# Kernel optimization log

Hardware: AMD Instinct MI355X
Metric: run time of the kernel (lower is better)

The kernel has to match this reference:

```python
import jax, jax.numpy as jnp
import numpy as np

B, S, F_DIM, FILT = 4096, 41, 128, 128
EPS_BN = 1e-5
EPS_SQ = 1e-21


def squash(v):
    n = jnp.linalg.norm(v, axis=-1, keepdims=True)
    return (1.0 - 1.0 / (jnp.exp(n) + EPS_SQ)) * (v / (n + EPS_SQ))


def position_linear(x, Wstack, bstack, window):
    # x: [B,S,F]; Wstack: [S, window*F, FILT]; bstack: [S, FILT]
    p = window // 2
    Bq, Sq, Fq = x.shape
    xp = jnp.pad(x, ((0, 0), (p, p), (0, 0)))
    idx = jnp.arange(Sq)[:, None] + jnp.arange(window)[None, :]  # [S, window]
    xw = xp[:, idx, :].reshape(Bq, Sq, window * Fq)
    return jax.nn.relu(jnp.einsum('bsf,sfo->bso', xw, Wstack) + bstack[None])


def batchnorm(x, g, b, axes):
    mu = jnp.mean(x, axis=axes, keepdims=True)
    var = jnp.var(x, axis=axes, keepdims=True)
    shape = [1] * x.ndim
    shape[1] = x.shape[1]
    return (x - mu) * jax.lax.rsqrt(var + EPS_BN) * g.reshape(shape) + b.reshape(shape)


def conv1d(x, w, groups=1):
    # x: [N,C,L], w: [O, C//groups, K], padding same (k=3, pad=1)
    return jax.lax.conv_general_dilated(
        x, w, window_strides=(1,), padding=[(1, 1)],
        dimension_numbers=('NCH', 'OIH', 'NCH'), feature_group_count=groups)


def setup_inputs() -> dict:
    key = jax.random.key(0)
    ks = jax.random.split(key, 16)
    sc = lambda fan_in: 1.0 / np.sqrt(fan_in)
    d = {}
    d['x'] = jax.random.randint(ks[0], (B, S), 0, 4, dtype=jnp.int32)
    d['emb'] = jax.random.normal(ks[1], (4, F_DIM), dtype=jnp.float32)
    for i, w in enumerate([3, 5, 7]):
        fin = w * F_DIM
        d[f'W{w}'] = jax.random.uniform(ks[2 + i], (S, fin, FILT), jnp.float32, -sc(fin), sc(fin))
        d[f'b{w}'] = jnp.zeros((S, FILT), jnp.float32)
    d['conv1_w'] = jax.random.uniform(ks[5], (64, 41, 3), jnp.float32, -sc(41 * 3), sc(41 * 3))
    d['conv1_b'] = jnp.zeros((64,), jnp.float32)
    d['bn_g'] = jnp.ones((64,), jnp.float32)
    d['bn_b'] = jnp.zeros((64,), jnp.float32)
    d['caps_w'] = jax.random.uniform(ks[6], (64, 32, 3), jnp.float32, -sc(32 * 3), sc(32 * 3))
    d['caps_b'] = jnp.zeros((64,), jnp.float32)
    d['route_W'] = jax.random.normal(ks[7], (2, 64, F_DIM), jnp.float32)
    d['route_b'] = jnp.zeros((2, 64, 1), jnp.float32)
    d['fc1_w'] = jax.random.uniform(ks[8], (F_DIM, 64), jnp.float32, -sc(F_DIM), sc(F_DIM))
    d['bn1_g'] = jnp.ones((2,), jnp.float32)
    d['bn1_b'] = jnp.zeros((2,), jnp.float32)
    d['fc2_w'] = jax.random.uniform(ks[9], (64, 32), jnp.float32, -sc(64), sc(64))
    d['bn2_g'] = jnp.ones((2,), jnp.float32)
    d['bn2_b'] = jnp.zeros((2,), jnp.float32)
    d['fc3_w'] = jax.random.uniform(ks[10], (32, 1), jnp.float32, -sc(32), sc(32))
    return d


def reference(x, emb, W3, b3, W5, b5, W7, b7, conv1_w, conv1_b, bn_g, bn_b,
              caps_w, caps_b, route_W, route_b,
              fc1_w, bn1_g, bn1_b, fc2_w, bn2_g, bn2_b, fc3_w):
    h = emb[x]                                    # [B,41,128]
    h = position_linear(h, W3, b3, 3)
    h = position_linear(h, W5, b5, 5)
    h = position_linear(h, W7, b7, 7)             # [B,41,128]
    h = conv1d(h, conv1_w) + conv1_b[None, :, None]  # [B,64,128]
    h = jax.nn.relu(batchnorm(h, bn_g, bn_b, axes=(0, 2)))
    h = conv1d(h, caps_w, groups=2) + caps_b[None, :, None]
    h = squash(h)                                 # [B,64,128]
    # Routing layer
    u = h[:, None, :, :] * route_W[None]          # [B,2,64,128]
    c = jnp.sum(u * u, axis=-1, keepdims=True) / jnp.sqrt(128.0)  # [B,2,64,1]
    c = jax.nn.softmax(c, axis=-1)                # softmax over size-1 axis -> ones
    c = c + route_b[None]
    s = squash(jnp.sum(u * c, axis=-2))           # [B,2,128]
    # FC head
    pair = s[:, :, None, :] + s[:, None, :, :]    # [B,2,2,128]
    y = jnp.max(pair, axis=1)                     # [B,2,128]
    y = jax.nn.relu(batchnorm(y @ fc1_w, bn1_g, bn1_b, axes=(0, 2)))
    y = jax.nn.relu(batchnorm(y @ fc2_w, bn2_g, bn2_b, axes=(0, 2)))
    y = jax.nn.sigmoid(y @ fc3_w)                 # [B,2,1]
    return jnp.max(y, axis=1)                     # [B,1]
```

## Files before the change

kernel.cpp:

```cpp
#include <hip/hip_runtime.h>
#include <cstdint>

typedef unsigned short u16;
typedef unsigned int   u32;
typedef __attribute__((ext_vector_type(8))) short bf16x8;
typedef __attribute__((ext_vector_type(4))) float f32x4;

#define DEVFN static __device__ __forceinline__

constexpr int B  = 4096;
constexpr int SQ = 41;

DEVFN float bf2f(u16 v) { return __uint_as_float(((u32)v) << 16); }
DEVFN u16 f2bf(float f) {
  u32 u = __float_as_uint(f);
  u += 0x7fffu + ((u >> 16) & 1u);
  return (u16)(u >> 16);
}
DEVFN u32 pack2(float a, float b) { return (u32)f2bf(a) | ((u32)f2bf(b) << 16); }

DEVFN void gload16(const void* g, void* l) {
  __builtin_amdgcn_global_load_lds(
      (const __attribute__((address_space(1))) unsigned int*)g,
      (__attribute__((address_space(3))) unsigned int*)l, 16, 0, 0);
}

__global__ void k_pack(const float* __restrict__ cw, const float* __restrict__ cpw,
                       const float* __restrict__ rW, const float* __restrict__ rb,
                       u16* __restrict__ wpk, u16* __restrict__ cpk,
                       u16* __restrict__ rwp) {
  int i = blockIdx.x * 256 + threadIdx.x;
  if (i < 12288) {
    int tt = i >> 12, rem = i & 4095, o = rem >> 6, c = rem & 63;
    float v = (c < 41) ? cw[(o * 41 + c) * 3 + tt] : 0.f;
    wpk[(tt * 64 + o) * 64 + (c ^ ((o & 7) << 3))] = f2bf(v);
  } else if (i < 18432) {
    int k = i - 12288;
    int tt = k >> 11, rem = k & 2047, o = rem >> 5, c = rem & 31;
    cpk[(tt * 64 + o) * 32 + (c ^ ((o & 3) << 3))] = f2bf(cpw[(o * 32 + c) * 3 + tt]);
  } else if (i < 34816) {
    int k = i - 18432;
    rwp[k] = f2bf(rW[k] * (1.f + rb[k >> 7]));
  }
}

__global__ void k_combo(const int* __restrict__ x, int* __restrict__ combo) {
  int i = blockIdx.x * 256 + threadIdx.x;
  if (i >= B * SQ) return;
  int b = i / SQ, s = i - b * SQ;
  const int* xb = x + b * SQ;
  int d0 = (s > 0) ? xb[s - 1] : 4;
  int d1 = xb[s];
  int d2 = (s < SQ - 1) ? xb[s + 1] : 4;
  combo[i] = d0 * 25 + d1 * 5 + d2;
}

__global__ void k_gmat(const float* __restrict__ emb, const float* __restrict__ W3,
                       float* __restrict__ G) {
  int s = blockIdx.x / 3, ww = blockIdx.x % 3;
  int o = threadIdx.x;
  const float* Ws = W3 + ((size_t)s * 384 + ww * 128) * 128;
  float a0 = 0.f, a1 = 0.f, a2 = 0.f, a3 = 0.f;
  for (int f = 0; f < 128; ++f) {
    float wg = Ws[(size_t)f * 128 + o];
    a0 = fmaf(emb[f], wg, a0);
    a1 = fmaf(emb[128 + f], wg, a1);
    a2 = fmaf(emb[256 + f], wg, a2);
    a3 = fmaf(emb[384 + f], wg, a3);
  }
  float* Gp = G + ((size_t)(s * 3 + ww) * 5) * 128 + o;
  Gp[0] = a0; Gp[128] = a1; Gp[256] = a2; Gp[384] = a3; Gp[512] = 0.f;
}

__global__ void k_t1(const float* __restrict__ G, const float* __restrict__ b3,
                     u16* __restrict__ t1b) {
  int i = blockIdx.x * 256 + threadIdx.x;
  int f = i & 127, v = (i >> 7) & 127, s = i >> 14;
  u16 out = 0;
  if (v < 125) {
    int d0 = v / 25, r = v % 25;
    int d1 = r / 5, d2 = r % 5;
    float acc = b3[s * 128 + f]
        + G[((size_t)(s * 3 + 0) * 5 + d0) * 128 + f]
        + G[((size_t)(s * 3 + 1) * 5 + d1) * 128 + f]
        + G[((size_t)(s * 3 + 2) * 5 + d2) * 128 + f];
    out = f2bf(fmaxf(acc, 0.f));
  }
  t1b[i] = out;
}

__global__ __launch_bounds__(256) void k_w5t(const float* __restrict__ W5,
                                             u16* __restrict__ w5t) {
  __shared__ float tile[64][65];
  const int sw = blockIdx.z;
  const int s = sw / 5, w = sw % 5;
  const int f0 = blockIdx.x * 64;
  const int o0 = blockIdx.y * 64;
  const int t = threadIdx.x;
  const float* Ws = W5 + ((size_t)s * 640 + w * 128) * 128;
  #pragma unroll
  for (int i = 0; i < 16; ++i) {
    int idx = t + i * 256;
    int fl = idx >> 6, ol = idx & 63;
    tile[fl][ol] = Ws[(size_t)(f0 + fl) * 128 + o0 + ol];
  }
  __syncthreads();
  #pragma unroll
  for (int i = 0; i < 16; ++i) {
    int idx = t + i * 256;
    int ol = idx >> 6, fl = idx & 63;
    w5t[((size_t)sw * 128 + o0 + ol) * 128 + f0 + fl] = f2bf(tile[fl][ol]);
  }
}

__global__ __launch_bounds__(256) void k_t2_mfma(const u16* __restrict__ t1b,
                                                 const u16* __restrict__ w5t,
                                                 u16* __restrict__ t2) {
  __shared__ u16 As[2][8192];
  __shared__ u16 Bs[2][8192];
  const int sw = blockIdx.x;
  const int s = sw / 5, w5 = sw % 5;
  const int tw = s + w5 - 2;
  if (tw < 0 || tw >= SQ) return;
  const int t = threadIdx.x;
  const int lane = t & 63, w = t >> 6;
  const int wr = w >> 1, wc = w & 1;
  const int lcol = lane & 15, qk = lane >> 4;

  const u16* abase = t1b + (size_t)tw * 128 * 128;
  const u16* bbase = w5t + (size_t)sw * 128 * 128;
  #pragma unroll
  for (int h = 0; h < 2; ++h) {
    #pragma unroll
    for (int it = 0; it < 4; ++it) {
      const int L = it * 4096 + t * 16;
      const int r = L >> 7, g = (L >> 4) & 7;
      const int gs = g ^ (r & 7);
      gload16(abase + (size_t)r * 128 + h * 64 + gs * 8,
              (char*)As[h] + it * 4096 + w * 1024);
      gload16(bbase + (size_t)r * 128 + h * 64 + gs * 8,
              (char*)Bs[h] + it * 4096 + w * 1024);
    }
  }
  __syncthreads();

  f32x4 acc[4][4];
  #pragma unroll
  for (int i = 0; i < 4; ++i)
    #pragma unroll
    for (int j = 0; j < 4; ++j) acc[i][j] = (f32x4){0.f, 0.f, 0.f, 0.f};

  #pragma unroll
  for (int h = 0; h < 2; ++h) {
    #pragma unroll
    for (int kk = 0; kk < 2; ++kk) {
      const int gk = kk * 4 + qk;
      bf16x8 av[4], bv[4];
      #pragma unroll
      for (int m = 0; m < 4; ++m) {
        const int zr = wr * 64 + m * 16 + lcol;
        av[m] = *reinterpret_cast<const bf16x8*>(&As[h][zr * 64 + ((gk ^ (zr & 7)) << 3)]);
      }
      #pragma unroll
      for (int n = 0; n < 4; ++n) {
        const int br = wc * 64 + n * 16 + lcol;
        bv[n] = *reinterpret_cast<const bf16x8*>(&Bs[h][br * 64 + ((gk ^ (br & 7)) << 3)]);
      }
      #pragma unroll
      for (int m = 0; m < 4; ++m)
        #pragma unroll
        for (int n = 0; n < 4; ++n)
          acc[m][n] = __builtin_amdgcn_mfma_f32_16x16x32_bf16(av[m], bv[n], acc[m][n], 0, 0, 0);
    }
  }

  u16* dst = t2 + (size_t)sw * 125 * 128;
  const int rq = (lane >> 4) * 4;
  #pragma unroll
  for (int n = 0; n < 4; ++n) {
    const int o = wc * 64 + n * 16 + lcol;
    #pragma unroll
    for (int m = 0; m < 4; ++m) {
      #pragma unroll
      for (int rg = 0; rg < 4; ++rg) {
        const int row = wr * 64 + m * 16 + rq + rg;
        if (row < 125) dst[(size_t)row * 128 + o] = f2bf(acc[m][n][rg]);
      }
    }
  }
}

__global__ __launch_bounds__(256) void k_h2(const u16* __restrict__ t2,
                                            const int* __restrict__ combo,
                                            const float* __restrict__ b5,
                                            u16* __restrict__ h2) {
  const int i = blockIdx.x * 256 + threadIdx.x;
  const int o8 = (i & 15) * 8;
  const int rid = i >> 4;
  const int s = rid >> 12, b = rid & 4095;
  float acc[8];
  {
    float4 b0 = *reinterpret_cast<const float4*>(b5 + s * 128 + o8);
    float4 b1 = *reinterpret_cast<const float4*>(b5 + s * 128 + o8 + 4);
    acc[0] = b0.x; acc[1] = b0.y; acc[2] = b0.z; acc[3] = b0.w;
    acc[4] = b1.x; acc[5] = b1.y; acc[6] = b1.z; acc[7] = b1.w;
  }
  const int* cb = combo + b * SQ;
  #pragma unroll
  for (int ww = 0; ww < 5; ++ww) {
    const int t = s + ww - 2;
    if (0 <= t && t < SQ) {
      const int c = cb[t];
      uint4 raw = *reinterpret_cast<const uint4*>(
          t2 + ((size_t)(s * 5 + ww) * 125 + c) * 128 + o8);
      acc[0] += __uint_as_float(raw.x << 16);
      acc[1] += __uint_as_float(raw.x & 0xffff0000u);
      acc[2] += __uint_as_float(raw.y << 16);
      acc[3] += __uint_as_float(raw.y & 0xffff0000u);
      acc[4] += __uint_as_float(raw.z << 16);
      acc[5] += __uint_as_float(raw.z & 0xffff0000u);
      acc[6] += __uint_as_float(raw.w << 16);
      acc[7] += __uint_as_float(raw.w & 0xffff0000u);
    }
  }
  uint4 pk;
  pk.x = pack2(fmaxf(acc[0], 0.f), fmaxf(acc[1], 0.f));
  pk.y = pack2(fmaxf(acc[2], 0.f), fmaxf(acc[3], 0.f));
  pk.z = pack2(fmaxf(acc[4], 0.f), fmaxf(acc[5], 0.f));
  pk.w = pack2(fmaxf(acc[6], 0.f), fmaxf(acc[7], 0.f));
  *reinterpret_cast<uint4*>(h2 + ((size_t)b * SQ + s) * 128 + o8) = pk;
}

__global__ __launch_bounds__(256) void k_w7t(const float* __restrict__ W7,
                                             u16* __restrict__ w7t) {
  __shared__ float tile[64][65];
  const int s = blockIdx.z;
  const int k0 = blockIdx.x * 64;
  const int o0 = blockIdx.y * 64;
  const int t = threadIdx.x;
  #pragma unroll
  for (int i = 0; i < 16; ++i) {
    int idx = t + i * 256;
    int kl = idx >> 6, ol = idx & 63;
    tile[kl][ol] = W7[((size_t)s * 896 + k0 + kl) * 128 + o0 + ol];
  }
  __syncthreads();
  #pragma unroll
  for (int i = 0; i < 16; ++i) {
    int idx = t + i * 256;
    int ol = idx >> 6, kl = idx & 63;
    w7t[((size_t)s * 128 + o0 + ol) * 896 + k0 + kl] = f2bf(tile[kl][ol]);
  }
}

__global__ __launch_bounds__(256) void k_gemm7_mfma(const u16* __restrict__ h2,
                                                    const u16* __restrict__ w7t,
                                                    const float* __restrict__ b7,
                                                    u16* __restrict__ h3) {
  __shared__ u16 As[2][8192];
  __shared__ u16 Bs[2][8192];
  const int s  = blockIdx.y;
  const int b0 = blockIdx.x * 128;
  const int t  = threadIdx.x;
  const int lane = t & 63, w = t >> 6;
  const int wr = w >> 1, wc = w & 1;
  const int lcol = lane & 15, qk = lane >> 4;

  f32x4 acc[4][4];
  #pragma unroll
  for (int i = 0; i < 4; ++i)
    #pragma unroll
    for (int j = 0; j < 4; ++j) acc[i][j] = (f32x4){0.f, 0.f, 0.f, 0.f};

  const u16* wbase = w7t + (size_t)s * 128 * 896;

  auto stage = [&](int kt, int bi) -> int {
    const int k0 = kt * 64;
    const int ww = k0 >> 7, tr = s + ww - 3, kf0 = k0 & 127;
    int issued = 0;
    if (0 <= tr && tr < SQ) {
      #pragma unroll
      for (int it = 0; it < 4; ++it) {
        const int L = it * 4096 + t * 16;
        const int r = L >> 7;
        const int g = (L >> 4) & 7;
        const int gs = g ^ (r & 7);
        gload16(h2 + ((size_t)(b0 + r) * SQ + tr) * 128 + kf0 + gs * 8,
                (char*)As[bi] + it * 4096 + w * 1024);
      }
      issued += 4;
    } else {
      #pragma unroll
      for (int it = 0; it < 4; ++it)
        *reinterpret_cast<uint4*>((char*)As[bi] + it * 4096 + t * 16) =
            make_uint4(0u, 0u, 0u, 0u);
    }
    #pragma unroll
    for (int it = 0; it < 4; ++it) {
      const int L = it * 4096 + t * 16;
      const int o = L >> 7;
      const int g = (L >> 4) & 7;
      const int gs = g ^ (o & 7);
      gload16(wbase + (size_t)o * 896 + k0 + gs * 8,
              (char*)Bs[bi] + it * 4096 + w * 1024);
    }
    return issued + 4;
  };

  stage(0, 0);

  for (int kt = 0; kt < 14; ++kt) {
    const int cur = kt & 1;
    int ni = 0;
    if (kt < 13) ni = stage(kt + 1, cur ^ 1);
    if (ni == 8)      asm volatile("s_waitcnt vmcnt(8) lgkmcnt(0)" ::: "memory");
    else if (ni == 4) asm volatile("s_waitcnt vmcnt(4) lgkmcnt(0)" ::: "memory");
    else              asm volatile("s_waitcnt vmcnt(0) lgkmcnt(0)" ::: "memory");
    __builtin_amdgcn_sched_barrier(0);
    __builtin_amdgcn_s_barrier();
    __builtin_amdgcn_sched_barrier(0);

    const u16* Ac = As[cur];
    const u16* Bc = Bs[cur];
    #pragma unroll
    for (int kk = 0; kk < 2; ++kk) {
      const int gk = kk * 4 + qk;
      bf16x8 av[4], bv[4];
      #pragma unroll
      for (int m = 0; m < 4; ++m) {
        const int zr = wr * 64 + m * 16 + lcol;
        av[m] = *reinterpret_cast<const bf16x8*>(Ac + zr * 64 + ((gk ^ (zr & 7)) << 3));
      }
      #pragma unroll
      for (int n = 0; n < 4; ++n) {
        const int br = wc * 64 + n * 16 + lcol;
        bv[n] = *reinterpret_cast<const bf16x8*>(Bc + br * 64 + ((gk ^ (br & 7)) << 3));
      }
      #pragma unroll
      for (int m = 0; m < 4; ++m)
        #pragma unroll
        for (int n = 0; n < 4; ++n)
          acc[m][n] = __builtin_amdgcn_mfma_f32_16x16x32_bf16(av[m], bv[n], acc[m][n], 0, 0, 0);
    }
    __builtin_amdgcn_sched_barrier(0);
    __builtin_amdgcn_s_barrier();
  }

  const int rq = (lane >> 4) * 4;
  #pragma unroll
  for (int n = 0; n < 4; ++n) {
    const int o = wc * 64 + n * 16 + lcol;
    const float bias = b7[s * 128 + o];
    #pragma unroll
    for (int m = 0; m < 4; ++m) {
      #pragma unroll
      for (int rg = 0; rg < 4; ++rg) {
        const int row = b0 + wr * 64 + m * 16 + rq + rg;
        h3[((size_t)row * SQ + s) * 128 + o] = f2bf(fmaxf(acc[m][n][rg] + bias, 0.f));
      }
    }
  }
}

constexpr int NBC = 8;
__global__ __launch_bounds__(256) void k_conv1(const u16* __restrict__ h3,
                                               const u16* __restrict__ wpk,
                                               const float* __restrict__ cb,
                                               u16* __restrict__ c1T,
                                               float2* __restrict__ part) {
  __shared__ u16 zs[2][6144];
  __shared__ u16 zt[130 * 64];
  __shared__ u16 wl[3 * 64 * 64];
  __shared__ float2 red[4][64];
  const int b0 = blockIdx.x * NBC;
  const int t = threadIdx.x;
  const int lane = t & 63, wv = t >> 6;
  const int r = lane & 15, kq = (lane >> 4) * 8, q = lane >> 4;

  #pragma unroll
  for (int it = 0; it < 6; ++it)
    gload16(wpk + ((size_t)it * 256 + t) * 8, (char*)wl + it * 4096 + wv * 1024);
  #pragma unroll
  for (int it = 0; it < 3; ++it)
    gload16(h3 + (size_t)b0 * (SQ * 128) + ((size_t)it * 256 + t) * 8,
            (char*)zs[0] + it * 4096 + wv * 1024);
  if (t < 64) zt[t] = 0;
  else if (t < 128) zt[129 * 64 + t - 64] = 0;
  __syncthreads();

  for (int i = 0; i < NBC; ++i) {
    const int b = b0 + i;
    const int cur = i & 1;

    {
      const int l = t & 127, jb = (t >> 7) * 32;
      const int sw = ((l + 1) & 7) << 3;
      u16* dst = zt + (l + 1) * 64;
      const u16* srcz = zs[cur];
      #pragma unroll
      for (int j = 0; j < 32; ++j) {
        int c = (jb + j + l) & 63;
        dst[c ^ sw] = (c < 41) ? srcz[c * 128 + l] : (u16)0;
      }
    }
    if (i + 1 < NBC) {
      #pragma unroll
      for (int it = 0; it < 3; ++it)
        gload16(h3 + (size_t)(b + 1) * (SQ * 128) + ((size_t)it * 256 + t) * 8,
                (char*)zs[cur ^ 1] + it * 4096 + wv * 1024);
    }
    asm volatile("s_waitcnt lgkmcnt(0)" ::: "memory");
    __builtin_amdgcn_sched_barrier(0);
    __builtin_amdgcn_s_barrier();
    __builtin_amdgcn_sched_barrier(0);

    f32x4 acc[2][4];
    #pragma unroll
    for (int m = 0; m < 2; ++m)
      #pragma unroll
      for (int n = 0; n < 4; ++n) acc[m][n] = (f32x4){0.f, 0.f, 0.f, 0.f};
    #pragma unroll
    for (int tt = 0; tt < 3; ++tt) {
      #pragma unroll
      for (int kk = 0; kk < 2; ++kk) {
        const int kof = kk * 32 + kq;
        bf16x8 av[2], bv[4];
        #pragma unroll
        for (int m = 0; m < 2; ++m) {
          const int zr = wv * 32 + m * 16 + r + tt;
          av[m] = *reinterpret_cast<const bf16x8*>(zt + zr * 64 + (kof ^ ((zr & 7) << 3)));
        }
        #pragma unroll
        for (int n = 0; n < 4; ++n) {
          const int o = n * 16 + r;
          bv[n] = *reinterpret_cast<const bf16x8*>(wl + (tt * 64 + o) * 64 + (kof ^ ((o & 7) << 3)));
        }
        #pragma unroll
        for (int m = 0; m < 2; ++m)
          #pragma unroll
          for (int n = 0; n < 4; ++n)
            acc[m][n] = __builtin_amdgcn_mfma_f32_16x16x32_bf16(av[m], bv[n], acc[m][n], 0, 0, 0);
      }
    }

    u16* outb = c1T + (size_t)b * 8192;
    #pragma unroll
    for (int n = 0; n < 4; ++n) {
      const int o = n * 16 + r;
      const float bias = cb[o];
      float s1 = 0.f, s2 = 0.f;
      #pragma unroll
      for (int m = 0; m < 2; ++m) {
        #pragma unroll
        for (int rg = 0; rg < 4; ++rg) {
          float v = acc[m][n][rg] + bias;
          s1 += v; s2 += v * v;
          outb[(wv * 32 + m * 16 + q * 4 + rg) * 64 + o] = f2bf(v);
        }
      }
      s1 += __shfl_xor(s1, 16); s1 += __shfl_xor(s1, 32);
      s2 += __shfl_xor(s2, 16); s2 += __shfl_xor(s2, 32);
      if (lane < 16) red[wv][n * 16 + lane] = make_float2(s1, s2);
    }
    __syncthreads();
    if (t < 64) {
      float S = red[0][t].x + red[1][t].x + red[2][t].x + red[3][t].x;
      float Q = red[0][t].y + red[1][t].y + red[2][t].y + red[3][t].y;
      part[(size_t)t * B + b] = make_float2(S, Q);
    }
    __syncthreads();
  }
}

__global__ void k_bnfin(const float2* __restrict__ part, const float* __restrict__ g,
                        const float* __restrict__ bb, float* __restrict__ scale,
                        float* __restrict__ shift) {
  int o = blockIdx.x;
  float s = 0.f, q = 0.f;
  for (int i = threadIdx.x; i < B; i += 256) {
    float2 p = part[(size_t)o * B + i];
    s += p.x; q += p.y;
  }
  #pragma unroll
  for (int off = 32; off; off >>= 1) { s += __shfl_down(s, off); q += __shfl_down(q, off); }
  __shared__ float rs[4], rq[4];
  int wv = threadIdx.x >> 6, ln = threadIdx.x & 63;
  if (ln == 0) { rs[wv] = s; rq[wv] = q; }
  __syncthreads();
  if (threadIdx.x == 0) {
    float S = rs[0] + rs[1] + rs[2] + rs[3];
    float Q = rq[0] + rq[1] + rq[2] + rq[3];
    const float n = (float)B * 128.f;
    float mu = S / n, var = Q / n - mu * mu;
    float sc = g[o] * rsqrtf(var + 1e-5f);
    scale[o] = sc; shift[o] = bb[o] - mu * sc;
  }
}

constexpr int NB = 8;
__global__ __launch_bounds__(256) void k_caps(const u16* __restrict__ c1T,
                                              const float* __restrict__ scale,
                                              const float* __restrict__ shift,
                                              const u16* __restrict__ cpk,
                                              const float* __restrict__ cpb,
                                              const u16* __restrict__ rwp,
                                              const float* __restrict__ f1,
                                              float* __restrict__ y1,
                                              float2* __restrict__ ppy1) {
  __shared__ u16 zt[130 * 64];
  __shared__ u16 wl[3 * 64 * 32];
  __shared__ float f1l[128 * 64];
  __shared__ float red[4][64];
  __shared__ float fl[64];
  __shared__ float sc_s[64], sh_s[64];
  __shared__ float red2[4][2];
  __shared__ float yl[2][128];
  __shared__ float pt[128];
  const int b0 = blockIdx.x * NB;
  const int t = threadIdx.x;
  const int lane = t & 63, wv = t >> 6;
  const int r = lane & 15, kq = (lane >> 4) * 8, q = lane >> 4;
  float ysum = 0.f, ysq = 0.f;

  #pragma unroll
  for (int it = 0; it < 3; ++it)
    gload16(cpk + ((size_t)it * 256 + t) * 8, (char*)wl + it * 4096 + wv * 1024);
  #pragma unroll
  for (int it = 0; it < 8; ++it)
    gload16(f1 + ((size_t)it * 256 + t) * 4, (char*)f1l + it * 4096 + wv * 1024);
  if (t < 64) { sc_s[t] = scale[t]; sh_s[t] = shift[t]; }
  if (t < 64) zt[t] = 0;
  else if (t < 128) zt[129 * 64 + t - 64] = 0;

  uint4 raw[4], rawn[4];
  {
    const u16* src = c1T + (size_t)b0 * 8192;
    #pragma unroll
    for (int p = 0; p < 4; ++p)
      raw[p] = *reinterpret_cast<const uint4*>(src + ((size_t)t + p * 256) * 8);
  }

  for (int i = 0; i < NB; ++i) {
    const int b = b0 + i;
    __syncthreads();

    #pragma unroll
    for (int p = 0; p < 4; ++p) {
      int idx = t + p * 256;
      int l = idx >> 3, c0 = (idx & 7) * 8;
      float vv[8];
      vv[0] = __uint_as_float(raw[p].x << 16); vv[1] = __uint_as_float(raw[p].x & 0xffff0000u);
      vv[2] = __uint_as_float(raw[p].y << 16); vv[3] = __uint_as_float(raw[p].y & 0xffff0000u);
      vv[4] = __uint_as_float(raw[p].z << 16); vv[5] = __uint_as_float(raw[p].z & 0xffff0000u);
      vv[6] = __uint_as_float(raw[p].w << 16); vv[7] = __uint_as_float(raw[p].w & 0xffff0000u);
      float a0 = fmaxf(fmaf(vv[0], sc_s[c0 + 0], sh_s[c0 + 0]), 0.f);
      float a1 = fmaxf(fmaf(vv[1], sc_s[c0 + 1], sh_s[c0 + 1]), 0.f);
      float a2 = fmaxf(fmaf(vv[2], sc_s[c0 + 2], sh_s[c0 + 2]), 0.f);
      float a3 = fmaxf(fmaf(vv[3], sc_s[c0 + 3], sh_s[c0 + 3]), 0.f);
      float a4 = fmaxf(fmaf(vv[4], sc_s[c0 + 4], sh_s[c0 + 4]), 0.f);
      float a5 = fmaxf(fmaf(vv[5], sc_s[c0 + 5], sh_s[c0 + 5]), 0.f);
      float a6 = fmaxf(fmaf(vv[6], sc_s[c0 + 6], sh_s[c0 + 6]), 0.f);
      float a7 = fmaxf(fmaf(vv[7], sc_s[c0 + 7], sh_s[c0 + 7]), 0.f);
      uint4 pk;
      pk.x = pack2(a0, a1); pk.y = pack2(a2, a3);
      pk.z = pack2(a4, a5); pk.w = pack2(a6, a7);
      *reinterpret_cast<uint4*>(zt + (l + 1) * 64 + (c0 ^ (((l + 1) & 7) << 3))) = pk;
    }
    if (i + 1 < NB) {
      const u16* srcn = c1T + (size_t)(b + 1) * 8192;
      #pragma unroll
      for (int p = 0; p < 4; ++p)
        rawn[p] = *reinterpret_cast<const uint4*>(srcn + ((size_t)t + p * 256) * 8);
    }
    __syncthreads();

    f32x4 acc[2][4];
    #pragma unroll
    for (int m = 0; m < 2; ++m)
      #pragma unroll
      for (int n = 0; n < 4; ++n) acc[m][n] = (f32x4){0.f, 0.f, 0.f, 0.f};
    #pragma unroll
    for (int tt = 0; tt < 3; ++tt) {
      bf16x8 av[2][2], bv[4];
      #pragma unroll
      for (int m = 0; m < 2; ++m) {
        const int zr = wv * 32 + m * 16 + r + tt;
        const int sw = (zr & 7) << 3;
        av[m][0] = *reinterpret_cast<const bf16x8*>(zt + zr * 64 + (kq ^ sw));
        av[m][1] = *reinterpret_cast<const bf16x8*>(zt + zr * 64 + ((32 + kq) ^ sw));
      }
      #pragma unroll
      for (int n = 0; n < 4; ++n) {
        const int o = n * 16 + r;
        bv[n] = *reinterpret_cast<const bf16x8*>(wl + (tt * 64 + o) * 32 + (kq ^ ((o & 3) << 3)));
      }
      #pragma unroll
      for (int m = 0; m < 2; ++m)
        #pragma unroll
        for (int n = 0; n < 4; ++n)
          acc[m][n] = __builtin_amdgcn_mfma_f32_16x16x32_bf16(av[m][n >> 1], bv[n], acc[m][n], 0, 0, 0);
    }

    #pragma unroll
    for (int n = 0; n < 4; ++n) {
      const int o = n * 16 + r;
      const float bias = cpb[o];
      float s2 = 0.f;
      #pragma unroll
      for (int m = 0; m < 2; ++m) {
        #pragma unroll
        for (int rg = 0; rg < 4; ++rg) {
          float v = acc[m][n][rg] + bias;
          acc[m][n][rg] = v;
          s2 += v * v;
        }
      }
      s2 += __shfl_xor(s2, 16); s2 += __shfl_xor(s2, 32);
      if (lane < 16) red[wv][n * 16 + lane] = s2;
    }
    __syncthreads();
    if (t < 64) {
      float S = red[0][t] + red[1][t] + red[2][t] + red[3][t];
      float nn = sqrtf(S);
      fl[t] = (1.f - 1.f / (expf(nn) + 1e-21f)) / (nn + 1e-21f);
    }
    __syncthreads();

    float s0[2][4], s1[2][4];
    #pragma unroll
    for (int m = 0; m < 2; ++m)
      #pragma unroll
      for (int rg = 0; rg < 4; ++rg) { s0[m][rg] = 0.f; s1[m][rg] = 0.f; }
    #pragma unroll
    for (int n = 0; n < 4; ++n) {
      const int o = n * 16 + r;
      const float fact = fl[o];
      #pragma unroll
      for (int m = 0; m < 2; ++m) {
        const int l0 = wv * 32 + m * 16 + q * 4;
        uint2 rw0 = *reinterpret_cast<const uint2*>(rwp + (size_t)o * 128 + l0);
        uint2 rw1 = *reinterpret_cast<const uint2*>(rwp + (size_t)(64 + o) * 128 + l0);
        #pragma unroll
        for (int rg = 0; rg < 4; ++rg) {
          float v = acc[m][n][rg] * fact;
          u32 w0w = (rg < 2) ? rw0.x : rw0.y;
          u32 w1w = (rg < 2) ? rw1.x : rw1.y;
          float w0 = __uint_as_float((rg & 1) ? (w0w & 0xffff0000u) : (w0w << 16));
          float w1 = __uint_as_float((rg & 1) ? (w1w & 0xffff0000u) : (w1w << 16));
          s0[m][rg] = fmaf(v, w0, s0[m][rg]);
          s1[m][rg] = fmaf(v, w1, s1[m][rg]);
        }
      }
    }
    #pragma unroll
    for (int m = 0; m < 2; ++m)
      #pragma unroll
      for (int rg = 0; rg < 4; ++rg) {
        #pragma unroll
        for (int off = 1; off <= 8; off <<= 1) {
          s0[m][rg] += __shfl_xor(s0[m][rg], off);
          s1[m][rg] += __shfl_xor(s1[m][rg], off);
        }
      }
    float n0 = 0.f, n1 = 0.f;
    #pragma unroll
    for (int m = 0; m < 2; ++m)
      #pragma unroll
      for (int rg = 0; rg < 4; ++rg) {
        n0 = fmaf(s0[m][rg], s0[m][rg], n0);
        n1 = fmaf(s1[m][rg], s1[m][rg], n1);
      }
    n0 += __shfl_xor(n0, 16); n0 += __shfl_xor(n0, 32);
    n1 += __shfl_xor(n1, 16); n1 += __shfl_xor(n1, 32);
    if (lane == 0) { red2[wv][0] = n0; red2[wv][1] = n1; }
    __syncthreads();
    {
      float t0 = red2[0][0] + red2[1][0] + red2[2][0] + red2[3][0];
      float t1 = red2[0][1] + red2[1][1] + red2[2][1] + red2[3][1];
      float nn0 = sqrtf(t0), nn1 = sqrtf(t1);
      float fa0 = (1.f - 1.f / (expf(nn0) + 1e-21f)) / (nn0 + 1e-21f);
      float fa1 = (1.f - 1.f / (expf(nn1) + 1e-21f)) / (nn1 + 1e-21f);
      if (r == 0) {
        #pragma unroll
        for (int m = 0; m < 2; ++m)
          #pragma unroll
          for (int rg = 0; rg < 4; ++rg) {
            float v0 = s0[m][rg] * fa0, v1 = s1[m][rg] * fa1;
            float mx = fmaxf(v0, v1);
            int l = wv * 32 + m * 16 + q * 4 + rg;
            yl[0][l] = v0 + mx;
            yl[1][l] = v1 + mx;
          }
      }
    }
    __syncthreads();

    {
      const int h = t >> 7, idx = t & 127;
      const int jj = idx >> 6, qq = idx & 63;
      float a = 0.f;
      const float* yrow = &yl[jj][h * 64];
      const float* frow = f1l + (h * 64) * 64 + qq;
      #pragma unroll 8
      for (int tt = 0; tt < 64; ++tt)
        a = fmaf(yrow[tt], frow[tt * 64], a);
      if (h == 1) pt[idx] = a;
      __syncthreads();
      float val = 0.f;
      if (h == 0) {
        val = a + pt[idx];
        y1[((size_t)b * 2 + jj) * 64 + qq] = val;
      }
      ysum += val; ysq += val * val;
    }

    #pragma unroll
    for (int p = 0; p < 4; ++p) raw[p] = rawn[p];
  }

  #pragma unroll
  for (int off = 32; off; off >>= 1) {
    ysum += __shfl_down(ysum, off);
    ysq  += __shfl_down(ysq, off);
  }
  __syncthreads();
  if (lane == 0) { red2[wv][0] = ysum; red2[wv][1] = ysq; }
  __syncthreads();
  if (t == 0) ppy1[blockIdx.x] = make_float2(red2[0][0] + red2[2][0],
                                             red2[0][1] + red2[2][1]);
  if (t == 1) ppy1[512 + blockIdx.x] = make_float2(red2[1][0] + red2[3][0],
                                                   red2[1][1] + red2[3][1]);
}

__global__ void k_bnstat_fin(const float2* __restrict__ pp, const float* __restrict__ g,
                             const float* __restrict__ bb, float* __restrict__ scale,
                             float* __restrict__ shift, int perShift, int nparts) {
  const int jj = blockIdx.x;
  float s = 0.f, q = 0.f;
  for (int i = threadIdx.x; i < nparts; i += 256) {
    float2 p = pp[jj * nparts + i];
    s += p.x; q += p.y;
  }
  #pragma unroll
  for (int off = 32; off; off >>= 1) { s += __shfl_down(s, off); q += __shfl_down(q, off); }
  __shared__ float rs[4], rq[4];
  int wv = threadIdx.x >> 6, ln = threadIdx.x & 63;
  if (ln == 0) { rs[wv] = s; rq[wv] = q; }
  __syncthreads();
  if (threadIdx.x == 0) {
    float S = rs[0] + rs[1] + rs[2] + rs[3];
    float Q = rq[0] + rq[1] + rq[2] + rq[3];
    float fn = (float)(B << perShift);
    float mu = S / fn, var = Q / fn - mu * mu;
    float sc = g[jj] * rsqrtf(var + 1e-5f);
    scale[jj] = sc; shift[jj] = bb[jj] - mu * sc;
  }
}

__global__ void k_fc2(const float* __restrict__ y1, const float* __restrict__ sc1,
                      const float* __restrict__ sh1, const float* __restrict__ f2,
                      float* __restrict__ y2, float2* __restrict__ ppy2) {
  __shared__ float2 r2[8];
  int t = threadIdx.x;
  int b = blockIdx.x * 4 + (t >> 6);
  int jj = (t >> 5) & 1, r = t & 31;
  float sc = sc1[jj], sh = sh1[jj];
  const float* yb = y1 + (size_t)b * 128 + jj * 64;
  float acc = 0.f;
  for (int q = 0; q < 64; ++q) {
    float v = fmaxf(fmaf(yb[q], sc, sh), 0.f);
    acc = fmaf(v, f2[q * 32 + r], acc);
  }
  y2[(size_t)b * 64 + jj * 32 + r] = acc;
  float s = acc, q2 = acc * acc;
  #pragma unroll
  for (int off = 16; off; off >>= 1) { s += __shfl_down(s, off); q2 += __shfl_down(q2, off); }
  if ((t & 31) == 0) r2[t >> 5] = make_float2(s, q2);
  __syncthreads();
  if (t == 0) ppy2[blockIdx.x] =
      make_float2(r2[0].x + r2[2].x + r2[4].x + r2[6].x,
                  r2[0].y + r2[2].y + r2[4].y + r2[6].y);
  if (t == 1) ppy2[1024 + blockIdx.x] =
      make_float2(r2[1].x + r2[3].x + r2[5].x + r2[7].x,
                  r2[1].y + r2[3].y + r2[5].y + r2[7].y);
}

__global__ void k_head(const float* __restrict__ y2, const float* __restrict__ sc2,
                       const float* __restrict__ sh2, const float* __restrict__ f3,
                       float* __restrict__ out) {
  int b = blockIdx.x * 256 + threadIdx.x;
  if (b >= B) return;
  const float* yb = y2 + (size_t)b * 64;
  float c0 = sc2[0], d0 = sh2[0], c1v = sc2[1], d1 = sh2[1];
  float a0 = 0.f, a1 = 0.f;
  for (int r = 0; r < 32; ++r) {
    float w = f3[r];
    a0 = fmaf(fmaxf(fmaf(yb[r], c0, d0), 0.f), w, a0);
    a1 = fmaf(fmaxf(fmaf(yb[32 + r], c1v, d1), 0.f), w, a1);
  }
  float s0 = 1.f / (1.f + expf(-a0));
  float s1 = 1.f / (1.f + expf(-a1));
  out[b] = fmaxf(s0, s1);
}

constexpr size_t SZ_H2    = (size_t)B * SQ * 128 * 2;
constexpr size_t SZ_C1    = (size_t)B * 64 * 128 * 2;
constexpr size_t OFF_H2   = 0;
constexpr size_t OFF_W5T  = 0;
constexpr size_t OFF_H3   = SZ_H2;
constexpr size_t R1       = 2 * SZ_H2;
constexpr size_t OFF_G    = R1;
constexpr size_t OFF_T1   = OFF_G + 314880;
constexpr size_t OFF_T2   = OFF_T1 + 2624000;
constexpr size_t OFF_CMB  = OFF_T2 + 6560000;
constexpr size_t OFF_W7T  = OFF_CMB + 671744;
constexpr size_t OFF_C1   = R1;
constexpr size_t R2       = R1 + SZ_C1;
constexpr size_t OFF_PART = R2;
constexpr size_t OFF_Y1   = OFF_PART + 2097152;
constexpr size_t OFF_Y2   = OFF_Y1 + 2097152;
constexpr size_t OFF_SM   = OFF_Y2 + 1048576;
constexpr size_t OFF_WPK  = OFF_SM + 1024;
constexpr size_t OFF_CPK  = OFF_WPK + 24576;
constexpr size_t OFF_RWP  = OFF_CPK + 12288;

extern "C" void kernel_launch(void* const* d_in, const int* in_sizes, int n_in,
                              void* d_out, int out_size, void* d_ws, size_t ws_size,
                              hipStream_t stream) {
  const int*   x   = (const int*)d_in[0];
  const float* emb = (const float*)d_in[1];
  const float* W3  = (const float*)d_in[2];
  const float* b3  = (const float*)d_in[3];
  const float* W5  = (const float*)d_in[4];
  const float* b5  = (const float*)d_in[5];
  const float* W7  = (const float*)d_in[6];
  const float* b7  = (const float*)d_in[7];
  const float* c1w = (const float*)d_in[8];
  const float* c1b = (const float*)d_in[9];
  const float* bng = (const float*)d_in[10];
  const float* bnb = (const float*)d_in[11];
  const float* cpw = (const float*)d_in[12];
  const float* cpb = (const float*)d_in[13];
  const float* rW  = (const float*)d_in[14];
  const float* rb  = (const float*)d_in[15];
  const float* f1  = (const float*)d_in[16];
  const float* g1  = (const float*)d_in[17];
  const float* bb1 = (const float*)d_in[18];
  const float* f2  = (const float*)d_in[19];
  const float* g2  = (const float*)d_in[20];
  const float* bb2 = (const float*)d_in[21];
  const float* f3  = (const float*)d_in[22];

  char* wsb = (char*)d_ws;
  u16*    h2p   = (u16*)(wsb + OFF_H2);
  u16*    w5tp  = (u16*)(wsb + OFF_W5T);
  u16*    h3p   = (u16*)(wsb + OFF_H3);
  float*  Gp    = (float*)(wsb + OFF_G);
  u16*    t1p   = (u16*)(wsb + OFF_T1);
  u16*    t2p   = (u16*)(wsb + OFF_T2);
  int*    cmbp  = (int*)(wsb + OFF_CMB);
  u16*    w7tp  = (u16*)(wsb + OFF_W7T);
  u16*    c1p   = (u16*)(wsb + OFF_C1);
  float2* partp = (float2*)(wsb + OFF_PART);
  float2* ppy1  = partp;
  float2* ppy2  = partp + 2048;
  float*  y1p   = (float*)(wsb + OFF_Y1);
  float*  y2p   = (float*)(wsb + OFF_Y2);
  float*  scp   = (float*)(wsb + OFF_SM);
  float*  shp   = scp + 64;
  float*  sc1p  = shp + 64;
  float*  sh1p  = sc1p + 2;
  float*  sc2p  = sh1p + 2;
  float*  sh2p  = sc2p + 2;
  u16*    wpkp  = (u16*)(wsb + OFF_WPK);
  u16*    cpkp  = (u16*)(wsb + OFF_CPK);
  u16*    rwpp  = (u16*)(wsb + OFF_RWP);

  k_pack<<<136, 256, 0, stream>>>(c1w, cpw, rW, rb, wpkp, cpkp, rwpp);
  k_combo<<<(B * SQ + 255) / 256, 256, 0, stream>>>(x, cmbp);
  k_w5t<<<dim3(2, 2, SQ * 5), 256, 0, stream>>>(W5, w5tp);
  k_w7t<<<dim3(14, 2, SQ), 256, 0, stream>>>(W7, w7tp);
  k_gmat<<<SQ * 3, 128, 0, stream>>>(emb, W3, Gp);
  k_t1<<<SQ * 128 * 128 / 256, 256, 0, stream>>>(Gp, b3, t1p);
  k_t2_mfma<<<SQ * 5, 256, 0, stream>>>(t1p, w5tp, t2p);
  k_h2<<<(B * SQ * 16) / 256, 256, 0, stream>>>(t2p, cmbp, b5, h2p);
  k_gemm7_mfma<<<dim3(32, SQ), 256, 0, stream>>>(h2p, w7tp, b7, h3p);
  k_conv1<<<B / NBC, 256, 0, stream>>>(h3p, wpkp, c1b, c1p, partp);
  k_bnfin<<<64, 256, 0, stream>>>(partp, bng, bnb, scp, shp);
  k_caps<<<B / NB, 256, 0, stream>>>(c1p, scp, shp, cpkp, cpb, rwpp, f1, y1p, ppy1);
  k_bnstat_fin<<<2, 256, 0, stream>>>(ppy1, g1, bb1, sc1p, sh1p, 6, 512);
  k_fc2<<<B / 4, 256, 0, stream>>>(y1p, sc1p, sh1p, f2, y2p, ppy2);
  k_bnstat_fin<<<2, 256, 0, stream>>>(ppy2, g2, bb2, sc2p, sh2p, 5, 1024);
  k_head<<<B / 256, 256, 0, stream>>>(y2p, sc2p, sh2p, f3, (float*)d_out);
}
```

Measured before the change: 216.3 us.

## Merge prep kernels, fuse t1 into t2 GEMM, fold BN finalize into consumers

```diff
diff --git a/kernel.cpp b/kernel.cpp
--- a/kernel.cpp
+++ b/kernel.cpp
@@ -25,95 +25,101 @@
       (__attribute__((address_space(3))) unsigned int*)l, 16, 0, 0);
 }
 
-__global__ void k_pack(const float* __restrict__ cw, const float* __restrict__ cpw,
-                       const float* __restrict__ rW, const float* __restrict__ rb,
-                       u16* __restrict__ wpk, u16* __restrict__ cpk,
-                       u16* __restrict__ rwp) {
-  int i = blockIdx.x * 256 + threadIdx.x;
-  if (i < 12288) {
-    int tt = i >> 12, rem = i & 4095, o = rem >> 6, c = rem & 63;
-    float v = (c < 41) ? cw[(o * 41 + c) * 3 + tt] : 0.f;
-    wpk[(tt * 64 + o) * 64 + (c ^ ((o & 7) << 3))] = f2bf(v);
-  } else if (i < 18432) {
-    int k = i - 12288;
-    int tt = k >> 11, rem = k & 2047, o = rem >> 5, c = rem & 31;
-    cpk[(tt * 64 + o) * 32 + (c ^ ((o & 3) << 3))] = f2bf(cpw[(o * 32 + c) * 3 + tt]);
-  } else if (i < 34816) {
-    int k = i - 18432;
-    rwp[k] = f2bf(rW[k] * (1.f + rb[k >> 7]));
-  }
-}
-
-__global__ void k_combo(const int* __restrict__ x, int* __restrict__ combo) {
-  int i = blockIdx.x * 256 + threadIdx.x;
-  if (i >= B * SQ) return;
-  int b = i / SQ, s = i - b * SQ;
-  const int* xb = x + b * SQ;
-  int d0 = (s > 0) ? xb[s - 1] : 4;
-  int d1 = xb[s];
-  int d2 = (s < SQ - 1) ? xb[s + 1] : 4;
-  combo[i] = d0 * 25 + d1 * 5 + d2;
-}
-
-__global__ void k_gmat(const float* __restrict__ emb, const float* __restrict__ W3,
-                       float* __restrict__ G) {
-  int s = blockIdx.x / 3, ww = blockIdx.x % 3;
-  int o = threadIdx.x;
-  const float* Ws = W3 + ((size_t)s * 384 + ww * 128) * 128;
-  float a0 = 0.f, a1 = 0.f, a2 = 0.f, a3 = 0.f;
-  for (int f = 0; f < 128; ++f) {
-    float wg = Ws[(size_t)f * 128 + o];
-    a0 = fmaf(emb[f], wg, a0);
-    a1 = fmaf(emb[128 + f], wg, a1);
-    a2 = fmaf(emb[256 + f], wg, a2);
-    a3 = fmaf(emb[384 + f], wg, a3);
-  }
-  float* Gp = G + ((size_t)(s * 3 + ww) * 5) * 128 + o;
-  Gp[0] = a0; Gp[128] = a1; Gp[256] = a2; Gp[384] = a3; Gp[512] = 0.f;
-}
-
-__global__ void k_t1(const float* __restrict__ G, const float* __restrict__ b3,
-                     u16* __restrict__ t1b) {
-  int i = blockIdx.x * 256 + threadIdx.x;
-  int f = i & 127, v = (i >> 7) & 127, s = i >> 14;
-  u16 out = 0;
-  if (v < 125) {
-    int d0 = v / 25, r = v % 25;
-    int d1 = r / 5, d2 = r % 5;
-    float acc = b3[s * 128 + f]
-        + G[((size_t)(s * 3 + 0) * 5 + d0) * 128 + f]
-        + G[((size_t)(s * 3 + 1) * 5 + d1) * 128 + f]
-        + G[((size_t)(s * 3 + 2) * 5 + d2) * 128 + f];
-    out = f2bf(fmaxf(acc, 0.f));
-  }
-  t1b[i] = out;
-}
-
-__global__ __launch_bounds__(256) void k_w5t(const float* __restrict__ W5,
-                                             u16* __restrict__ w5t) {
+__global__ __launch_bounds__(256) void k_prep(
+    const float* __restrict__ cw, const float* __restrict__ cpw,
+    const float* __restrict__ rW, const float* __restrict__ rb,
+    u16* __restrict__ wpk, u16* __restrict__ cpk, u16* __restrict__ rwp,
+    const int* __restrict__ x, int* __restrict__ combo,
+    const float* __restrict__ W5, u16* __restrict__ w5t,
+    const float* __restrict__ W7, u16* __restrict__ w7t,
+    const float* __restrict__ emb, const float* __restrict__ W3,
+    float* __restrict__ G) {
   __shared__ float tile[64][65];
-  const int sw = blockIdx.z;
-  const int s = sw / 5, w = sw % 5;
-  const int f0 = blockIdx.x * 64;
-  const int o0 = blockIdx.y * 64;
+  const int blk = blockIdx.x;
   const int t = threadIdx.x;
-  const float* Ws = W5 + ((size_t)s * 640 + w * 128) * 128;
-  #pragma unroll
-  for (int i = 0; i < 16; ++i) {
-    int idx = t + i * 256;
-    int fl = idx >> 6, ol = idx & 63;
-    tile[fl][ol] = Ws[(size_t)(f0 + fl) * 128 + o0 + ol];
-  }
-  __syncthreads();
-  #pragma unroll
-  for (int i = 0; i < 16; ++i) {
-    int idx = t + i * 256;
-    int ol = idx >> 6, fl = idx & 63;
-    w5t[((size_t)sw * 128 + o0 + ol) * 128 + f0 + fl] = f2bf(tile[fl][ol]);
-  }
-}
-
-__global__ __launch_bounds__(256) void k_t2_mfma(const u16* __restrict__ t1b,
+
+  if (blk < 136) {
+    int i = blk * 256 + t;
+    if (i < 12288) {
+      int tt = i >> 12, rem = i & 4095, o = rem >> 6, c = rem & 63;
+      float v = (c < 41) ? cw[(o * 41 + c) * 3 + tt] : 0.f;
+      wpk[(tt * 64 + o) * 64 + (c ^ ((o & 7) << 3))] = f2bf(v);
+    } else if (i < 18432) {
+      int k = i - 12288;
+      int tt = k >> 11, rem = k & 2047, o = rem >> 5, c = rem & 31;
+      cpk[(tt * 64 + o) * 32 + (c ^ ((o & 3) << 3))] = f2bf(cpw[(o * 32 + c) * 3 + tt]);
+    } else if (i < 34816) {
+      int k = i - 18432;
+      rwp[k] = f2bf(rW[k] * (1.f + rb[k >> 7]));
+    }
+  } else if (blk < 793) {
+    int i = (blk - 136) * 256 + t;
+    if (i < B * SQ) {
+      int b = i / SQ, s = i - b * SQ;
+      const int* xb = x + b * SQ;
+      int d0 = (s > 0) ? xb[s - 1] : 4;
+      int d1 = xb[s];
+      int d2 = (s < SQ - 1) ? xb[s + 1] : 4;
+      combo[i] = d0 * 25 + d1 * 5 + d2;
+    }
+  } else if (blk < 1613) {
+    int flat = blk - 793;
+    int sw = flat >> 2, r4 = flat & 3;
+    int f0 = (r4 & 1) * 64, o0 = (r4 >> 1) * 64;
+    int s = sw / 5, w = sw % 5;
+    const float* Ws = W5 + ((size_t)s * 640 + w * 128) * 128;
+    #pragma unroll
+    for (int i = 0; i < 16; ++i) {
+      int idx = t + i * 256;
+      int fl = idx >> 6, ol = idx & 63;
+      tile[fl][ol] = Ws[(size_t)(f0 + fl) * 128 + o0 + ol];
+    }
+    __syncthreads();
+    #pragma unroll
+    for (int i = 0; i < 16; ++i) {
+      int idx = t + i * 256;
+      int ol = idx >> 6, fl = idx & 63;
+      w5t[((size_t)sw * 128 + o0 + ol) * 128 + f0 + fl] = f2bf(tile[fl][ol]);
+    }
+  } else if (blk < 2761) {
+    int flat = blk - 1613;
+    int s = flat / 28, r28 = flat % 28;
+    int k0 = (r28 >> 1) * 64, o0 = (r28 & 1) * 64;
+    #pragma unroll
+    for (int i = 0; i < 16; ++i) {
+      int idx = t + i * 256;
+      int kl = idx >> 6, ol = idx & 63;
+      tile[kl][ol] = W7[((size_t)s * 896 + k0 + kl) * 128 + o0 + ol];
+    }
+    __syncthreads();
+    #pragma unroll
+    for (int i = 0; i < 16; ++i) {
+      int idx = t + i * 256;
+      int ol = idx >> 6, kl = idx & 63;
+      w7t[((size_t)s * 128 + o0 + ol) * 896 + k0 + kl] = f2bf(tile[kl][ol]);
+    }
+  } else {
+    int blk2 = blk - 2761;
+    int s = blk2 / 3, ww = blk2 % 3;
+    if (t < 128) {
+      const int o = t;
+      const float* Ws = W3 + ((size_t)s * 384 + ww * 128) * 128;
+      float a0 = 0.f, a1 = 0.f, a2 = 0.f, a3 = 0.f;
+      for (int f = 0; f < 128; ++f) {
+        float wg = Ws[(size_t)f * 128 + o];
+        a0 = fmaf(emb[f], wg, a0);
+        a1 = fmaf(emb[128 + f], wg, a1);
+        a2 = fmaf(emb[256 + f], wg, a2);
+        a3 = fmaf(emb[384 + f], wg, a3);
+      }
+      float* Gp = G + ((size_t)(s * 3 + ww) * 5) * 128 + o;
+      Gp[0] = a0; Gp[128] = a1; Gp[256] = a2; Gp[384] = a3; Gp[512] = 0.f;
+    }
+  }
+}
+
+__global__ __launch_bounds__(256) void k_t2_mfma(const float* __restrict__ G,
+                                                 const float* __restrict__ b3,
                                                  const u16* __restrict__ w5t,
                                                  u16* __restrict__ t2) {
   __shared__ u16 As[2][8192];
@@ -127,7 +133,6 @@
   const int wr = w >> 1, wc = w & 1;
   const int lcol = lane & 15, qk = lane >> 4;
 
-  const u16* abase = t1b + (size_t)tw * 128 * 128;
   const u16* bbase = w5t + (size_t)sw * 128 * 128;
   #pragma unroll
   for (int h = 0; h < 2; ++h) {
@@ -136,11 +141,31 @@
       const int L = it * 4096 + t * 16;
       const int r = L >> 7, g = (L >> 4) & 7;
       const int gs = g ^ (r & 7);
-      gload16(abase + (size_t)r * 128 + h * 64 + gs * 8,
-              (char*)As[h] + it * 4096 + w * 1024);
       gload16(bbase + (size_t)r * 128 + h * 64 + gs * 8,
               (char*)Bs[h] + it * 4096 + w * 1024);
     }
+  }
+  #pragma unroll
+  for (int p = 0; p < 8; ++p) {
+    int idx = t + p * 256;
+    int v = idx >> 4, hg = idx & 15;
+    int h = hg >> 3, gl = hg & 7;
+    int f0 = h * 64 + gl * 8;
+    uint4 pk = make_uint4(0u, 0u, 0u, 0u);
+    if (v < 125) {
+      int d0 = v / 25, rr = v % 25, d1 = rr / 5, d2 = rr % 5;
+      const float* g0 = G + ((size_t)(tw * 3 + 0) * 5 + d0) * 128 + f0;
+      const float* g1 = G + ((size_t)(tw * 3 + 1) * 5 + d1) * 128 + f0;
+      const float* g2 = G + ((size_t)(tw * 3 + 2) * 5 + d2) * 128 + f0;
+      const float* bb = b3 + tw * 128 + f0;
+      float vals[8];
+      #pragma unroll
+      for (int e = 0; e < 8; ++e)
+        vals[e] = fmaxf(bb[e] + g0[e] + g1[e] + g2[e], 0.f);
+      pk.x = pack2(vals[0], vals[1]); pk.y = pack2(vals[2], vals[3]);
+      pk.z = pack2(vals[4], vals[5]); pk.w = pack2(vals[6], vals[7]);
+    }
+    *reinterpret_cast<uint4*>(&As[h][v * 64 + ((gl ^ (v & 7)) << 3)]) = pk;
   }
   __syncthreads();
 
@@ -229,28 +254,6 @@
   pk.z = pack2(fmaxf(acc[4], 0.f), fmaxf(acc[5], 0.f));
   pk.w = pack2(fmaxf(acc[6], 0.f), fmaxf(acc[7], 0.f));
   *reinterpret_cast<uint4*>(h2 + ((size_t)b * SQ + s) * 128 + o8) = pk;
-}
-
-__global__ __launch_bounds__(256) void k_w7t(const float* __restrict__ W7,
-                                             u16* __restrict__ w7t) {
-  __shared__ float tile[64][65];
-  const int s = blockIdx.z;
-  const int k0 = blockIdx.x * 64;
-  const int o0 = blockIdx.y * 64;
-  const int t = threadIdx.x;
-  #pragma unroll
-  for (int i = 0; i < 16; ++i) {
-    int idx = t + i * 256;
-    int kl = idx >> 6, ol = idx & 63;
-    tile[kl][ol] = W7[((size_t)s * 896 + k0 + kl) * 128 + o0 + ol];
-  }
-  __syncthreads();
-  #pragma unroll
-  for (int i = 0; i < 16; ++i) {
-    int idx = t + i * 256;
-    int ol = idx >> 6, kl = idx & 63;
-    w7t[((size_t)s * 128 + o0 + ol) * 896 + k0 + kl] = f2bf(tile[kl][ol]);
-  }
 }
 
 __global__ __launch_bounds__(256) void k_gemm7_mfma(const u16* __restrict__ h2,
@@ -732,39 +735,47 @@
                                                    red2[1][1] + red2[3][1]);
 }
 
-__global__ void k_bnstat_fin(const float2* __restrict__ pp, const float* __restrict__ g,
-                             const float* __restrict__ bb, float* __restrict__ scale,
-                             float* __restrict__ shift, int perShift, int nparts) {
-  const int jj = blockIdx.x;
-  float s = 0.f, q = 0.f;
-  for (int i = threadIdx.x; i < nparts; i += 256) {
-    float2 p = pp[jj * nparts + i];
-    s += p.x; q += p.y;
-  }
-  #pragma unroll
-  for (int off = 32; off; off >>= 1) { s += __shfl_down(s, off); q += __shfl_down(q, off); }
-  __shared__ float rs[4], rq[4];
-  int wv = threadIdx.x >> 6, ln = threadIdx.x & 63;
-  if (ln == 0) { rs[wv] = s; rq[wv] = q; }
-  __syncthreads();
-  if (threadIdx.x == 0) {
-    float S = rs[0] + rs[1] + rs[2] + rs[3];
-    float Q = rq[0] + rq[1] + rq[2] + rq[3];
-    float fn = (float)(B << perShift);
-    float mu = S / fn, var = Q / fn - mu * mu;
-    float sc = g[jj] * rsqrtf(var + 1e-5f);
-    scale[jj] = sc; shift[jj] = bb[jj] - mu * sc;
-  }
-}
-
-__global__ void k_fc2(const float* __restrict__ y1, const float* __restrict__ sc1,
-                      const float* __restrict__ sh1, const float* __restrict__ f2,
-                      float* __restrict__ y2, float2* __restrict__ ppy2) {
+__global__ __launch_bounds__(256) void k_fc2(const float* __restrict__ y1,
+                                             const float2* __restrict__ ppy1,
+                                             const float* __restrict__ g1,
+                                             const float* __restrict__ bb1,
+                                             const float* __restrict__ f2,
+                                             float* __restrict__ y2,
+                                             float2* __restrict__ ppy2) {
   __shared__ float2 r2[8];
+  __shared__ float scs[2], shs[2];
+  __shared__ float r4[4][4];
   int t = threadIdx.x;
+  {
+    float s0 = 0.f, q0 = 0.f, s1 = 0.f, q1 = 0.f;
+    for (int i = t; i < 512; i += 256) {
+      float2 p0 = ppy1[i];       s0 += p0.x; q0 += p0.y;
+      float2 p1 = ppy1[512 + i]; s1 += p1.x; q1 += p1.y;
+    }
+    #pragma unroll
+    for (int off = 32; off; off >>= 1) {
+      s0 += __shfl_down(s0, off); q0 += __shfl_down(q0, off);
+      s1 += __shfl_down(s1, off); q1 += __shfl_down(q1, off);
+    }
+    int wv = t >> 6;
+    if ((t & 63) == 0) { r4[wv][0] = s0; r4[wv][1] = q0; r4[wv][2] = s1; r4[wv][3] = q1; }
+    __syncthreads();
+    if (t == 0) {
+      float fn = (float)B * 64.f;
+      float S0 = r4[0][0] + r4[1][0] + r4[2][0] + r4[3][0];
+      float Q0 = r4[0][1] + r4[1][1] + r4[2][1] + r4[3][1];
+      float S1 = r4[0][2] + r4[1][2] + r4[2][2] + r4[3][2];
+      float Q1 = r4[0][3] + r4[1][3] + r4[2][3] + r4[3][3];
+      float mu0 = S0 / fn, var0 = Q0 / fn - mu0 * mu0;
+      float mu1 = S1 / fn, var1 = Q1 / fn - mu1 * mu1;
+      scs[0] = g1[0] * rsqrtf(var0 + 1e-5f); shs[0] = bb1[0] - mu0 * scs[0];
+      scs[1] = g1[1] * rsqrtf(var1 + 1e-5f); shs[1] = bb1[1] - mu1 * scs[1];
+    }
+    __syncthreads();
+  }
   int b = blockIdx.x * 4 + (t >> 6);
   int jj = (t >> 5) & 1, r = t & 31;
-  float sc = sc1[jj], sh = sh1[jj];
+  float sc = scs[jj], sh = shs[jj];
   const float* yb = y1 + (size_t)b * 128 + jj * 64;
   float acc = 0.f;
   for (int q = 0; q < 64; ++q) {
@@ -785,13 +796,46 @@
                   r2[1].y + r2[3].y + r2[5].y + r2[7].y);
 }
 
-__global__ void k_head(const float* __restrict__ y2, const float* __restrict__ sc2,
-                       const float* __restrict__ sh2, const float* __restrict__ f3,
-                       float* __restrict__ out) {
-  int b = blockIdx.x * 256 + threadIdx.x;
+__global__ __launch_bounds__(256) void k_head(const float* __restrict__ y2,
+                                              const float2* __restrict__ ppy2,
+                                              const float* __restrict__ g2,
+                                              const float* __restrict__ bb2,
+                                              const float* __restrict__ f3,
+                                              float* __restrict__ out) {
+  __shared__ float scs[2], shs[2];
+  __shared__ float r4[4][4];
+  int t = threadIdx.x;
+  {
+    float s0 = 0.f, q0 = 0.f, s1 = 0.f, q1 = 0.f;
+    for (int i = t; i < 1024; i += 256) {
+      float2 p0 = ppy2[i];        s0 += p0.x; q0 += p0.y;
+      float2 p1 = ppy2[1024 + i]; s1 += p1.x; q1 += p1.y;
+    }
+    #pragma unroll
+    for (int off = 32; off; off >>= 1) {
+      s0 += __shfl_down(s0, off); q0 += __shfl_down(q0, off);
+      s1 += __shfl_down(s1, off); q1 += __shfl_down(q1, off);
+    }
+    int wv = t >> 6;
+    if ((t & 63) == 0) { r4[wv][0] = s0; r4[wv][1] = q0; r4[wv][2] = s1; r4[wv][3] = q1; }
+    __syncthreads();
+    if (t == 0) {
+      float fn = (float)B * 32.f;
+      float S0 = r4[0][0] + r4[1][0] + r4[2][0] + r4[3][0];
+      float Q0 = r4[0][1] + r4[1][1] + r4[2][1] + r4[3][1];
+      float S1 = r4[0][2] + r4[1][2] + r4[2][2] + r4[3][2];
+      float Q1 = r4[0][3] + r4[1][3] + r4[2][3] + r4[3][3];
+      float mu0 = S0 / fn, var0 = Q0 / fn - mu0 * mu0;
+      float mu1 = S1 / fn, var1 = Q1 / fn - mu1 * mu1;
+      scs[0] = g2[0] * rsqrtf(var0 + 1e-5f); shs[0] = bb2[0] - mu0 * scs[0];
+      scs[1] = g2[1] * rsqrtf(var1 + 1e-5f); shs[1] = bb2[1] - mu1 * scs[1];
+    }
+    __syncthreads();
+  }
+  int b = blockIdx.x * 256 + t;
   if (b >= B) return;
   const float* yb = y2 + (size_t)b * 64;
-  float c0 = sc2[0], d0 = sh2[0], c1v = sc2[1], d1 = sh2[1];
+  float c0 = scs[0], d0 = shs[0], c1v = scs[1], d1 = shs[1];
   float a0 = 0.f, a1 = 0.f;
   for (int r = 0; r < 32; ++r) {
     float w = f3[r];
@@ -810,8 +854,7 @@
 constexpr size_t OFF_H3   = SZ_H2;
 constexpr size_t R1       = 2 * SZ_H2;
 constexpr size_t OFF_G    = R1;
-constexpr size_t OFF_T1   = OFF_G + 314880;
-constexpr size_t OFF_T2   = OFF_T1 + 2624000;
+constexpr size_t OFF_T2   = OFF_G + 314880 + 2624000;
 constexpr size_t OFF_CMB  = OFF_T2 + 6560000;
 constexpr size_t OFF_W7T  = OFF_CMB + 671744;
 constexpr size_t OFF_C1   = R1;
@@ -856,7 +899,6 @@
   u16*    w5tp  = (u16*)(wsb + OFF_W5T);
   u16*    h3p   = (u16*)(wsb + OFF_H3);
   float*  Gp    = (float*)(wsb + OFF_G);
-  u16*    t1p   = (u16*)(wsb + OFF_T1);
   u16*    t2p   = (u16*)(wsb + OFF_T2);
   int*    cmbp  = (int*)(wsb + OFF_CMB);
   u16*    w7tp  = (u16*)(wsb + OFF_W7T);
@@ -868,28 +910,18 @@
   float*  y2p   = (float*)(wsb + OFF_Y2);
   float*  scp   = (float*)(wsb + OFF_SM);
   float*  shp   = scp + 64;
-  float*  sc1p  = shp + 64;
-  float*  sh1p  = sc1p + 2;
-  float*  sc2p  = sh1p + 2;
-  float*  sh2p  = sc2p + 2;
   u16*    wpkp  = (u16*)(wsb + OFF_WPK);
   u16*    cpkp  = (u16*)(wsb + OFF_CPK);
   u16*    rwpp  = (u16*)(wsb + OFF_RWP);
 
-  k_pack<<<136, 256, 0, stream>>>(c1w, cpw, rW, rb, wpkp, cpkp, rwpp);
-  k_combo<<<(B * SQ + 255) / 256, 256, 0, stream>>>(x, cmbp);
-  k_w5t<<<dim3(2, 2, SQ * 5), 256, 0, stream>>>(W5, w5tp);
-  k_w7t<<<dim3(14, 2, SQ), 256, 0, stream>>>(W7, w7tp);
-  k_gmat<<<SQ * 3, 128, 0, stream>>>(emb, W3, Gp);
-  k_t1<<<SQ * 128 * 128 / 256, 256, 0, stream>>>(Gp, b3, t1p);
-  k_t2_mfma<<<SQ * 5, 256, 0, stream>>>(t1p, w5tp, t2p);
+  k_prep<<<2884, 256, 0, stream>>>(c1w, cpw, rW, rb, wpkp, cpkp, rwpp,
+                                   x, cmbp, W5, w5tp, W7, w7tp, emb, W3, Gp);
+  k_t2_mfma<<<SQ * 5, 256, 0, stream>>>(Gp, b3, w5tp, t2p);
   k_h2<<<(B * SQ * 16) / 256, 256, 0, stream>>>(t2p, cmbp, b5, h2p);
   k_gemm7_mfma<<<dim3(32, SQ), 256, 0, stream>>>(h2p, w7tp, b7, h3p);
   k_conv1<<<B / NBC, 256, 0, stream>>>(h3p, wpkp, c1b, c1p, partp);
   k_bnfin<<<64, 256, 0, stream>>>(partp, bng, bnb, scp, shp);
   k_caps<<<B / NB, 256, 0, stream>>>(c1p, scp, shp, cpkp, cpb, rwpp, f1, y1p, ppy1);
-  k_bnstat_fin<<<2, 256, 0, stream>>>(ppy1, g1, bb1, sc1p, sh1p, 6, 512);
-  k_fc2<<<B / 4, 256, 0, stream>>>(y1p, sc1p, sh1p, f2, y2p, ppy2);
-  k_bnstat_fin<<<2, 256, 0, stream>>>(ppy2, g2, bb2, sc2p, sh2p, 5, 1024);
-  k_head<<<B / 256, 256, 0, stream>>>(y2p, sc2p, sh2p, f3, (float*)d_out);
-}
+  k_fc2<<<B / 4, 256, 0, stream>>>(y1p, ppy1, g1, bb1, f2, y2p, ppy2);
+  k_head<<<B / 256, 256, 0, stream>>>(y2p, ppy2, g2, bb2, f3, (float*)d_out);
+}
```

Measured after the change: 201.4 us. 1.07x faster.
